# Kernel tuning notes

Measured on AMD Instinct MI355X. Metric: run time of the kernel, lower is better.

## Reference

```python
import jax, jax.numpy as jnp
import numpy as np

# irreps: 256x0e + 128x1e + 64x2e + 32x3e
IRREPS = [(256, 0), (128, 1), (64, 2), (32, 3)]
EPS = 1e-5
N_GROUPS = len(IRREPS)          # 4 irrep groups
N_SCALAR_GROUPS = 1             # one contiguous 0e block
N_POINTS = 65536


def _build_indices():
    group_idx, irrep_idx, scalar_idx, scalar_grp = [], [], [], []
    off, ir, sg = 0, 0, 0
    for g, (n, l) in enumerate(IRREPS):
        d = 2 * l + 1
        group_idx += [g] * (n * d)
        for _ in range(n):
            irrep_idx += [ir] * d
            ir += 1
        if l == 0:
            scalar_idx += list(range(off, off + n))
            scalar_grp += [sg] * n
            sg += 1
        off += n * d
    return (np.array(group_idx, np.int32), np.array(irrep_idx, np.int32),
            np.array(scalar_idx, np.int32), np.array(scalar_grp, np.int32))


def setup_inputs() -> dict:
    key = jax.random.key(0)
    g_idx, i_idx, s_idx, s_grp = _build_indices()
    dim = g_idx.shape[0]          # 1184
    n_irreps = int(i_idx.max()) + 1   # 480
    scalar_dim = s_idx.shape[0]       # 256
    x = jax.random.normal(key, (N_POINTS, dim), dtype=jnp.float32)
    weight = jnp.ones((n_irreps,), dtype=jnp.float32)
    bias = jnp.zeros((scalar_dim,), dtype=jnp.float32)
    return {
        "x": x, "weight": weight, "bias": bias,
        "group_idx": jnp.asarray(g_idx), "irrep_idx": jnp.asarray(i_idx),
        "scalar_indices": jnp.asarray(s_idx), "scalar_group": jnp.asarray(s_grp),
    }


def reference(x, weight, bias, group_idx, irrep_idx, scalar_indices, scalar_group):
    dim = x.shape[-1]
    # --- subtract per-0e-group scalar mean ---
    scalar = x[:, scalar_indices]                                    # [N, S]
    sg_oh = jax.nn.one_hot(scalar_group, N_SCALAR_GROUPS, dtype=x.dtype)  # [S, Gs]
    sg_counts = sg_oh.sum(axis=0)                                    # [Gs]
    smean = (scalar @ sg_oh) / sg_counts                             # [N, Gs]
    smean_full = jnp.zeros_like(x).at[:, scalar_indices].set(smean[:, scalar_group])
    xc = x - smean_full
    # --- per irrep-group component variance ('component' normalization) ---
    g_oh = jax.nn.one_hot(group_idx, N_GROUPS, dtype=x.dtype)       # [dim, G]
    g_counts = g_oh.sum(axis=0)                                      # [G]
    var = (jnp.square(xc) @ g_oh) / g_counts                         # [N, G]
    rnorm = jax.lax.rsqrt(var + EPS)[:, group_idx]                   # [N, dim]
    # irrepwise scalar multiply by weight
    rnorm = rnorm * weight[irrep_idx]                                # [N, dim]
    out = xc * rnorm
    # affine bias on scalar (0e) components only
    bias_full = jnp.zeros((dim,), dtype=x.dtype).at[scalar_indices].set(bias)
    return out + bias_full
```

## Files before the change

kernel.cpp:

```cpp
#include <hip/hip_runtime.h>


#define DIM   1184
#define NF4   296
#define EPSV  1e-5f

__global__ __launch_bounds__(256) void eln_kernel(
    const float* __restrict__ x,
    const float* __restrict__ weight,
    const float* __restrict__ bias,
    float* __restrict__ out,
    int n_rows)
{
    const int wave = threadIdx.x >> 6;
    const int lane = threadIdx.x & 63;
    const int row  = blockIdx.x * 4 + wave;
    if (row >= n_rows) return;

    const float4* __restrict__ xr = (const float4*)(x + (size_t)row * DIM);
    float4* __restrict__ orow     = (float4*)(out + (size_t)row * DIM);

    float4 v[5];
    float ssum = 0.f, sq0 = 0.f, sq1 = 0.f, sq2 = 0.f, sq3 = 0.f;

#pragma unroll
    for (int it = 0; it < 5; ++it) {
        const int f4 = lane + it * 64;
        if (f4 < NF4) {
            float4 a = xr[f4];
            v[it] = a;
            const float s2 = a.x*a.x + a.y*a.y + a.z*a.z + a.w*a.w;
            if (f4 < 64)       { ssum += a.x + a.y + a.z + a.w; sq0 += s2; }
            else if (f4 < 160) { sq1 += s2; }
            else if (f4 < 240) { sq2 += s2; }
            else               { sq3 += s2; }
        }
    }

#pragma unroll
    for (int off = 32; off > 0; off >>= 1) {
        ssum += __shfl_xor(ssum, off);
        sq0  += __shfl_xor(sq0,  off);
        sq1  += __shfl_xor(sq1,  off);
        sq2  += __shfl_xor(sq2,  off);
        sq3  += __shfl_xor(sq3,  off);
    }

    const float m   = ssum * (1.f / 256.f);
    const float v0  = fmaxf(sq0 * (1.f / 256.f) - m * m, 0.f);
    const float rn0 = rsqrtf(v0 + EPSV);
    const float rn1 = rsqrtf(sq1 * (1.f / 384.f) + EPSV);
    const float rn2 = rsqrtf(sq2 * (1.f / 320.f) + EPSV);
    const float rn3 = rsqrtf(sq3 * (1.f / 224.f) + EPSV);

#pragma unroll
    for (int it = 0; it < 5; ++it) {
        const int f4 = lane + it * 64;
        if (f4 < NF4) {
            const float4 a = v[it];
            float4 o;
            const int e = f4 * 4;
            if (f4 < 64) {
                o.x = (a.x - m) * rn0 * weight[e + 0] + bias[e + 0];
                o.y = (a.y - m) * rn0 * weight[e + 1] + bias[e + 1];
                o.z = (a.z - m) * rn0 * weight[e + 2] + bias[e + 2];
                o.w = (a.w - m) * rn0 * weight[e + 3] + bias[e + 3];
            } else if (f4 < 160) {
                const int j = e - 256;
                o.x = a.x * rn1 * weight[256 + (j + 0) / 3];
                o.y = a.y * rn1 * weight[256 + (j + 1) / 3];
                o.z = a.z * rn1 * weight[256 + (j + 2) / 3];
                o.w = a.w * rn1 * weight[256 + (j + 3) / 3];
            } else if (f4 < 240) {
                const int j = e - 640;
                o.x = a.x * rn2 * weight[384 + (j + 0) / 5];
                o.y = a.y * rn2 * weight[384 + (j + 1) / 5];
                o.z = a.z * rn2 * weight[384 + (j + 2) / 5];
                o.w = a.w * rn2 * weight[384 + (j + 3) / 5];
            } else {
                const int j = e - 960;
                o.x = a.x * rn3 * weight[448 + (j + 0) / 7];
                o.y = a.y * rn3 * weight[448 + (j + 1) / 7];
                o.z = a.z * rn3 * weight[448 + (j + 2) / 7];
                o.w = a.w * rn3 * weight[448 + (j + 3) / 7];
            }
            orow[f4] = o;
        }
    }
}

extern "C" void kernel_launch(void* const* d_in, const int* in_sizes, int n_in,
                              void* d_out, int out_size, void* d_ws, size_t ws_size,
                              hipStream_t stream)
{
    const float* x      = (const float*)d_in[0];
    const float* weight = (const float*)d_in[1];
    const float* bias   = (const float*)d_in[2];
    float* out          = (float*)d_out;

    const int n_rows = in_sizes[0] / DIM;
    const int blocks = (n_rows + 3) / 4;
    eln_kernel<<<blocks, 256, 0, stream>>>(x, weight, bias, out, n_rows);
}
```

Measured before the change: 502.8 us.

## Use persistent waves with preloaded per-lane weights and nontemporal vector IO

Each wave now processes multiple rows in a grid-stride loop, launching one eighth as many blocks. Per-lane weight and bias vectors are gathered once into registers and reused across rows, which removes the per-element weight gathers and integer divisions from the inner loop. Row loads and stores use nontemporal builtins, and the group branching is replaced with lane-predicated selects. The cost is fewer waves in flight for hiding memory latency on a kernel bound by streaming bandwidth.

```diff
diff --git a/kernel.cpp b/kernel.cpp
--- a/kernel.cpp
+++ b/kernel.cpp
@@ -4,6 +4,13 @@
 #define DIM   1184
 #define NF4   296
 #define EPSV  1e-5f
+#define ROWS_PER_WAVE 8
+
+typedef float f4 __attribute__((ext_vector_type(4)));
+
+__device__ __forceinline__ float dot4(const f4 a) {
+    return a.x*a.x + a.y*a.y + a.z*a.z + a.w*a.w;
+}
 
 __global__ __launch_bounds__(256) void eln_kernel(
     const float* __restrict__ x,
@@ -12,79 +19,101 @@
     float* __restrict__ out,
     int n_rows)
 {
-    const int wave = threadIdx.x >> 6;
-    const int lane = threadIdx.x & 63;
-    const int row  = blockIdx.x * 4 + wave;
-    if (row >= n_rows) return;
+    const int wave    = threadIdx.x >> 6;
+    const int lane    = threadIdx.x & 63;
+    const int wave_id = blockIdx.x * 4 + wave;
+    const int n_waves = gridDim.x * 4;
 
-    const float4* __restrict__ xr = (const float4*)(x + (size_t)row * DIM);
-    float4* __restrict__ orow     = (float4*)(out + (size_t)row * DIM);
+    f4 w[5];
+#pragma unroll
+    for (int it = 0; it < 5; ++it) {
+        const int f4i = lane + it * 64;
+        float wt[4];
+#pragma unroll
+        for (int c = 0; c < 4; ++c) {
+            const int e = f4i * 4 + c;
+            int idx;
+            if (e < 256)      idx = e;
+            else if (e < 640) idx = 256 + (e - 256) / 3;
+            else if (e < 960) idx = 384 + (e - 640) / 5;
+            else              idx = 448 + (e - 960) / 7;
+            idx = idx < 479 ? idx : 479;
+            wt[c] = (f4i < NF4) ? weight[idx] : 0.f;
+        }
+        w[it].x = wt[0]; w[it].y = wt[1]; w[it].z = wt[2]; w[it].w = wt[3];
+    }
+    const f4 bb = ((const f4*)bias)[lane];
 
-    float4 v[5];
-    float ssum = 0.f, sq0 = 0.f, sq1 = 0.f, sq2 = 0.f, sq3 = 0.f;
+    for (int row = wave_id; row < n_rows; row += n_waves) {
+        const f4* __restrict__ xr = (const f4*)(x + (size_t)row * DIM);
+        f4* __restrict__ orow     = (f4*)(out + (size_t)row * DIM);
+
+        const f4 v0 = __builtin_nontemporal_load(xr + lane);
+        const f4 v1 = __builtin_nontemporal_load(xr + lane + 64);
+        const f4 v2 = __builtin_nontemporal_load(xr + lane + 128);
+        const f4 v3 = __builtin_nontemporal_load(xr + lane + 192);
+        f4 v4 = (f4){0.f, 0.f, 0.f, 0.f};
+        if (lane < 40) v4 = __builtin_nontemporal_load(xr + lane + 256);
+
+        float ssum = v0.x + v0.y + v0.z + v0.w;
+        float sq0  = dot4(v0);
+        const float s2_1 = dot4(v1);
+        const float s2_2 = dot4(v2);
+        const float s2_3 = dot4(v3);
+        const float s2_4 = dot4(v4);
+        float sq1 = s2_1 + ((lane < 32) ? s2_2 : 0.f);
+        float sq2 = ((lane < 32) ? 0.f : s2_2) + ((lane < 48) ? s2_3 : 0.f);
+        float sq3 = ((lane < 48) ? 0.f : s2_3) + s2_4;
 
 #pragma unroll
-    for (int it = 0; it < 5; ++it) {
-        const int f4 = lane + it * 64;
-        if (f4 < NF4) {
-            float4 a = xr[f4];
-            v[it] = a;
-            const float s2 = a.x*a.x + a.y*a.y + a.z*a.z + a.w*a.w;
-            if (f4 < 64)       { ssum += a.x + a.y + a.z + a.w; sq0 += s2; }
-            else if (f4 < 160) { sq1 += s2; }
-            else if (f4 < 240) { sq2 += s2; }
-            else               { sq3 += s2; }
+        for (int off = 32; off > 0; off >>= 1) {
+            ssum += __shfl_xor(ssum, off);
+            sq0  += __shfl_xor(sq0,  off);
+            sq1  += __shfl_xor(sq1,  off);
+            sq2  += __shfl_xor(sq2,  off);
+            sq3  += __shfl_xor(sq3,  off);
         }
-    }
 
-#pragma unroll
-    for (int off = 32; off > 0; off >>= 1) {
-        ssum += __shfl_xor(ssum, off);
-        sq0  += __shfl_xor(sq0,  off);
-        sq1  += __shfl_xor(sq1,  off);
-        sq2  += __shfl_xor(sq2,  off);
-        sq3  += __shfl_xor(sq3,  off);
-    }
+        const float m   = ssum * (1.f / 256.f);
+        const float v0v = fmaxf(sq0 * (1.f / 256.f) - m * m, 0.f);
+        const float rn0 = rsqrtf(v0v + EPSV);
+        const float rn1 = rsqrtf(sq1 * (1.f / 384.f) + EPSV);
+        const float rn2 = rsqrtf(sq2 * (1.f / 320.f) + EPSV);
+        const float rn3 = rsqrtf(sq3 * (1.f / 224.f) + EPSV);
+        const float rnA = (lane < 32) ? rn1 : rn2;
+        const float rnB = (lane < 48) ? rn2 : rn3;
 
-    const float m   = ssum * (1.f / 256.f);
-    const float v0  = fmaxf(sq0 * (1.f / 256.f) - m * m, 0.f);
-    const float rn0 = rsqrtf(v0 + EPSV);
-    const float rn1 = rsqrtf(sq1 * (1.f / 384.f) + EPSV);
-    const float rn2 = rsqrtf(sq2 * (1.f / 320.f) + EPSV);
-    const float rn3 = rsqrtf(sq3 * (1.f / 224.f) + EPSV);
+        f4 o;
+        o.x = (v0.x - m) * (rn0 * w[0].x) + bb.x;
+        o.y = (v0.y - m) * (rn0 * w[0].y) + bb.y;
+        o.z = (v0.z - m) * (rn0 * w[0].z) + bb.z;
+        o.w = (v0.w - m) * (rn0 * w[0].w) + bb.w;
+        __builtin_nontemporal_store(o, orow + lane);
 
-#pragma unroll
-    for (int it = 0; it < 5; ++it) {
-        const int f4 = lane + it * 64;
-        if (f4 < NF4) {
-            const float4 a = v[it];
-            float4 o;
-            const int e = f4 * 4;
-            if (f4 < 64) {
-                o.x = (a.x - m) * rn0 * weight[e + 0] + bias[e + 0];
-                o.y = (a.y - m) * rn0 * weight[e + 1] + bias[e + 1];
-                o.z = (a.z - m) * rn0 * weight[e + 2] + bias[e + 2];
-                o.w = (a.w - m) * rn0 * weight[e + 3] + bias[e + 3];
-            } else if (f4 < 160) {
-                const int j = e - 256;
-                o.x = a.x * rn1 * weight[256 + (j + 0) / 3];
-                o.y = a.y * rn1 * weight[256 + (j + 1) / 3];
-                o.z = a.z * rn1 * weight[256 + (j + 2) / 3];
-                o.w = a.w * rn1 * weight[256 + (j + 3) / 3];
-            } else if (f4 < 240) {
-                const int j = e - 640;
-                o.x = a.x * rn2 * weight[384 + (j + 0) / 5];
-                o.y = a.y * rn2 * weight[384 + (j + 1) / 5];
-                o.z = a.z * rn2 * weight[384 + (j + 2) / 5];
-                o.w = a.w * rn2 * weight[384 + (j + 3) / 5];
-            } else {
-                const int j = e - 960;
-                o.x = a.x * rn3 * weight[448 + (j + 0) / 7];
-                o.y = a.y * rn3 * weight[448 + (j + 1) / 7];
-                o.z = a.z * rn3 * weight[448 + (j + 2) / 7];
-                o.w = a.w * rn3 * weight[448 + (j + 3) / 7];
-            }
-            orow[f4] = o;
+        o.x = v1.x * (rn1 * w[1].x);
+        o.y = v1.y * (rn1 * w[1].y);
+        o.z = v1.z * (rn1 * w[1].z);
+        o.w = v1.w * (rn1 * w[1].w);
+        __builtin_nontemporal_store(o, orow + lane + 64);
+
+        o.x = v2.x * (rnA * w[2].x);
+        o.y = v2.y * (rnA * w[2].y);
+        o.z = v2.z * (rnA * w[2].z);
+        o.w = v2.w * (rnA * w[2].w);
+        __builtin_nontemporal_store(o, orow + lane + 128);
+
+        o.x = v3.x * (rnB * w[3].x);
+        o.y = v3.y * (rnB * w[3].y);
+        o.z = v3.z * (rnB * w[3].z);
+        o.w = v3.w * (rnB * w[3].w);
+        __builtin_nontemporal_store(o, orow + lane + 192);
+
+        if (lane < 40) {
+            o.x = v4.x * (rn3 * w[4].x);
+            o.y = v4.y * (rn3 * w[4].y);
+            o.z = v4.z * (rn3 * w[4].z);
+            o.w = v4.w * (rn3 * w[4].w);
+            __builtin_nontemporal_store(o, orow + lane + 256);
         }
     }
 }
@@ -99,6 +128,6 @@
     float* out          = (float*)d_out;
 
     const int n_rows = in_sizes[0] / DIM;
-    const int blocks = (n_rows + 3) / 4;
+    const int blocks = (n_rows + ROWS_PER_WAVE * 4 - 1) / (ROWS_PER_WAVE * 4);
     eln_kernel<<<blocks, 256, 0, stream>>>(x, weight, bias, out, n_rows);
 }
```

Result: no change. 498.1 us (-0.9%).
